# Performance work log

Hardware: AMD Instinct MI355X
Metric: run time of the kernel (lower is better)

The kernel has to match this reference:

```python
import jax, jax.numpy as jnp
import numpy as np

N = 32768      # total nodes
G = 64         # graphs
NPG = 512      # nodes per graph (equal-size graphs)
K = 256        # ceil(NPG * pooling_ratio), pooling_ratio=0.5
D = 256        # input_dim
H = 256        # hidden_dim
FD = 3 * H     # fusion dim
C = 10         # num_classes
E = 262144     # edges
EPS = 1e-5     # BatchNorm eps


def setup_inputs() -> dict:
    key = jax.random.key(0)
    ks = jax.random.split(key, 20)
    w = lambda k, s: jax.random.normal(k, s, jnp.float32) * 0.05
    inp = {
        'x': jax.random.normal(ks[0], (N, D), jnp.float32),
        'edge_index': jax.random.randint(ks[1], (2, E), 0, N, jnp.int64),
        'batch': (jnp.arange(N, dtype=jnp.int64) // NPG),
        'w_s1': w(ks[2], (D, H)), 'b_s1': jnp.zeros((H,), jnp.float32),
        'w_s21': w(ks[3], (D, H)), 'b_s21': jnp.zeros((H,), jnp.float32),
        'w_s22': w(ks[4], (H, H)), 'b_s22': jnp.zeros((H,), jnp.float32),
        'w_raw': w(ks[5], (D, H)), 'b_raw': jnp.zeros((H,), jnp.float32),
        'w_pos': w(ks[6], (FD, 1)), 'b_pos': jnp.zeros((1,), jnp.float32),
        'w_neg': w(ks[7], (FD, 1)), 'b_neg': jnp.zeros((1,), jnp.float32),
        'w_pool': w(ks[8], (FD, FD)), 'b_pool': jnp.zeros((FD,), jnp.float32),
        'w1': w(ks[9], (2 * FD, 256)), 'b1': jnp.zeros((256,), jnp.float32),
        'g1': jnp.ones((256,), jnp.float32), 'be1': jnp.zeros((256,), jnp.float32),
        'w2': w(ks[10], (256, 256)), 'b2': jnp.zeros((256,), jnp.float32),
        'g2': jnp.ones((256,), jnp.float32), 'be2': jnp.zeros((256,), jnp.float32),
        'w3': w(ks[11], (256, 256)), 'b3': jnp.zeros((256,), jnp.float32),
        'g3': jnp.ones((256,), jnp.float32), 'be3': jnp.zeros((256,), jnp.float32),
        'w4': w(ks[12], (256, C)), 'b4': jnp.zeros((C,), jnp.float32),
    }
    return inp


def _gcn(x, W, b, src, dst, dinv):
    # PyG GCNConv: linear, then sym-normalized aggregation with self-loops
    h = x @ W
    norm = dinv[src] * dinv[dst]
    agg = jax.ops.segment_sum(h[src] * norm[:, None], dst, num_segments=N)
    agg = agg + h * (dinv * dinv)[:, None]  # self-loop contribution
    return agg + b


def _bn(z, g, b):
    m = z.mean(0)
    v = z.var(0)  # biased, as torch BN training-mode normalization
    return (z - m) * jax.lax.rsqrt(v + EPS) * g + b


def _mlp(z, w1, b1, g1, be1, w2, b2, g2, be2, w3, b3, g3, be3, w4, b4):
    z = jax.nn.relu(_bn(z @ w1 + b1, g1, be1))  # dropout=identity (eval)
    idt = z
    o = jax.nn.relu(_bn(z @ w2 + b2, g2, be2))
    z = o + idt
    idt = z
    o = jax.nn.relu(_bn(z @ w3 + b3, g3, be3))
    z = o + idt
    return z @ w4 + b4


def _topk_mask(scores):
    # equal-size graphs -> per-graph top-k via one batched lax.top_k
    sg = scores.reshape(G, NPG)
    _, idx = jax.lax.top_k(sg, K)
    mask = jnp.zeros((G, NPG), bool).at[jnp.arange(G)[:, None], idx].set(True)
    return mask.reshape(-1)


def _readout(xt, mask):
    m = mask[:, None]
    xs = jnp.where(m, xt, 0.0).reshape(G, NPG, FD)
    mean_pool = xs.sum(1) / K
    mx = jnp.where(m, xt, -jnp.inf).reshape(G, NPG, FD).max(1)
    return jnp.concatenate([mean_pool, mx], axis=1)


def reference(x, edge_index, batch, w_s1, b_s1, w_s21, b_s21, w_s22, b_s22,
              w_raw, b_raw, w_pos, b_pos, w_neg, b_neg, w_pool, b_pool,
              w1, b1, g1, be1, w2, b2, g2, be2, w3, b3, g3, be3, w4, b4):
    src, dst = edge_index[0], edge_index[1]
    deg = jax.ops.segment_sum(jnp.ones_like(src, jnp.float32), dst, num_segments=N) + 1.0
    dinv = jax.lax.rsqrt(deg)
    lrelu = lambda z: jax.nn.leaky_relu(z, 0.01)

    h_s1 = lrelu(_gcn(x, w_s1, b_s1, src, dst, dinv))
    h_s2 = lrelu(_gcn(lrelu(_gcn(x, w_s21, b_s21, src, dst, dinv)), w_s22, b_s22, src, dst, dinv))
    h_raw = x @ w_raw + b_raw
    h_final = jnp.concatenate([h_s1, h_s2, h_raw], axis=1)  # [N, FD]

    score_pos = jax.nn.sigmoid(_gcn(h_final, w_pos, b_pos, src, dst, dinv)).reshape(-1)
    score_neg = jax.nn.sigmoid(_gcn(h_final, w_neg, b_neg, src, dst, dinv)).reshape(-1)

    xt = jax.nn.sigmoid(h_final @ w_pool + b_pool)  # pool_transform for all nodes; mask selects
    mask_pos = _topk_mask(score_pos)
    mask_neg = _topk_mask(score_neg)

    mlp = lambda e: _mlp(e, w1, b1, g1, be1, w2, b2, g2, be2, w3, b3, g3, be3, w4, b4)
    logits_pos = mlp(_readout(xt, mask_pos))
    probs_pos = jax.nn.softmax(logits_pos, axis=1)
    logits_neg = mlp(_readout(xt, mask_neg))
    probs_neg = jax.nn.softmax(logits_neg, axis=1)
    return (logits_pos, probs_pos, probs_neg, score_pos, score_neg, batch)
```

## Files before the change

kernel.cpp:

```cpp
#include <hip/hip_runtime.h>
#include <hip/hip_bf16.h>

#define N_NODES 32768
#define NGRAPH  64
#define NPG     512
#define TOPK    256
#define HID     256
#define FDIM    768
#define NEDGE   262144
#define NCLS    10
#define BN_EPS  1e-5f

#define IN_BF16 0
#define OUT_BF16 0

typedef __attribute__((ext_vector_type(8))) short short8;
typedef __attribute__((ext_vector_type(4))) float f32x4;

__device__ __forceinline__ float bf2f(unsigned short u) {
    return __uint_as_float(((unsigned)u) << 16);
}
__device__ __forceinline__ unsigned short f2bf(float f) {
    unsigned x = __float_as_uint(f);
    unsigned r = (x + 0x7fffu + ((x >> 16) & 1u)) >> 16;
    return (unsigned short)r;
}
__device__ __forceinline__ float in_ld(const void* p, size_t i) {
#if IN_BF16
    return bf2f(((const unsigned short*)p)[i]);
#else
    return ((const float*)p)[i];
#endif
}
__device__ __forceinline__ void st_out(void* o, size_t i, float v) {
#if OUT_BF16
    ((unsigned short*)o)[i] = f2bf(v);
#else
    ((float*)o)[i] = v;
#endif
}

__device__ __forceinline__ void async_cp16(const unsigned short* g, unsigned short* l) {
    __builtin_amdgcn_global_load_lds(
        (const __attribute__((address_space(1))) unsigned int*)g,
        (__attribute__((address_space(3))) unsigned int*)l, 16, 0, 0);
}

__device__ __forceinline__ void tile_swizzle(int& bm, int& bn) {
    int nx = gridDim.x;
    int L = blockIdx.y * nx + blockIdx.x;
    int xcd = L & 7;
    int j = L >> 3;
    bm = ((j / nx) * 8 + xcd) * 128;
    bn = (j % nx) * 128;
}

__global__ __launch_bounds__(256) void cvt_kernel(const float* __restrict__ in,
                                                  unsigned short* __restrict__ out, int n) {
    int i = blockIdx.x * 256 + threadIdx.x;
    if (i < n) out[i] = f2bf(in[i]);
}

__global__ __launch_bounds__(256) void cvt_t_kernel(const float* __restrict__ in,
                                                    unsigned short* __restrict__ out, int K, int N) {
    __shared__ unsigned short tile[32][33];
    int bk = blockIdx.x * 32, bn = blockIdx.y * 32;
    int tx = threadIdx.x & 31, ty = threadIdx.x >> 5;
#pragma unroll
    for (int i = 0; i < 32; i += 8)
        tile[ty + i][tx] = f2bf(in[(size_t)(bk + ty + i) * N + bn + tx]);
    __syncthreads();
#pragma unroll
    for (int i = 0; i < 32; i += 8)
        out[(size_t)(bn + ty + i) * K + bk + tx] = tile[tx][ty + i];
}

__global__ __launch_bounds__(256) void detect_kernel(const int* __restrict__ eb, int* __restrict__ flag) {
    int i = blockIdx.x * 256 + threadIdx.x;
    int v = eb[2 * (size_t)i + 1];
    unsigned long long b = __ballot(v != 0);
    if ((threadIdx.x & 63) == 0 && b)
        atomicAdd(flag, (int)__popcll(b));
}

__global__ __launch_bounds__(256) void hist_kernel(const int* __restrict__ eb, const int* __restrict__ flag,
                                                   int* __restrict__ deg) {
    int e = blockIdx.x * 256 + threadIdx.x;
    int st = (*flag == 0) ? 2 : 1;
    unsigned d = ((const unsigned*)eb)[(size_t)(NEDGE + e) * st] & (N_NODES - 1);
    atomicAdd(&deg[d], 1);
}

__global__ __launch_bounds__(256) void dinv_kernel(const int* __restrict__ deg, float* __restrict__ dinv) {
    int i = blockIdx.x * 256 + threadIdx.x;
    dinv[i] = rsqrtf((float)deg[i] + 1.0f);
}

__global__ __launch_bounds__(1024) void scan_kernel(const int* __restrict__ cnt, int* __restrict__ rowptr,
                                                    int* __restrict__ cursor) {
    __shared__ int part[1024];
    int t = threadIdx.x;
    int base = t * 32;
    int loc[32];
    int s = 0;
#pragma unroll
    for (int i = 0; i < 32; i++) { loc[i] = cnt[base + i]; s += loc[i]; }
    part[t] = s;
    __syncthreads();
    for (int off = 1; off < 1024; off <<= 1) {
        int v = (t >= off) ? part[t - off] : 0;
        __syncthreads();
        part[t] += v;
        __syncthreads();
    }
    int run = (t == 0) ? 0 : part[t - 1];
#pragma unroll
    for (int i = 0; i < 32; i++) {
        rowptr[base + i] = run;
        cursor[base + i] = run;
        run += loc[i];
    }
    if (t == 1023) rowptr[N_NODES] = run;
}

__global__ __launch_bounds__(256) void scatter_kernel(const int* __restrict__ eb, const int* __restrict__ flag,
                                                      int* __restrict__ cursor, int* __restrict__ srcs) {
    int e = blockIdx.x * 256 + threadIdx.x;
    int st = (*flag == 0) ? 2 : 1;
    unsigned s = ((const unsigned*)eb)[(size_t)e * st] & (N_NODES - 1);
    unsigned d = ((const unsigned*)eb)[(size_t)(NEDGE + e) * st] & (N_NODES - 1);
    int p = atomicAdd(&cursor[d], 1);
    srcs[p] = (int)s;
}

#define GEMM_CORE(K_)                                                           \
    __shared__ unsigned short As[128 * 64];                                     \
    __shared__ unsigned short Bs[128 * 64];                                     \
    const int tid = threadIdx.x;                                                \
    const int wave = tid >> 6;                                                  \
    const int lane = tid & 63;                                                  \
    int bm, bn;                                                                 \
    tile_swizzle(bm, bn);                                                       \
    const int wm = (wave >> 1) * 64;                                            \
    const int wn = (wave & 1) * 64;                                             \
    const int l15 = lane & 15;                                                  \
    const int q = lane >> 4;                                                    \
    f32x4 acc[4][4] = {};                                                       \
    const int srow = lane >> 3;                                                 \
    const int schunk = lane & 7;                                                \
    for (int k0 = 0; k0 < (K_); k0 += 64) {                                     \
        __syncthreads();                                                        \
        _Pragma("unroll")                                                       \
        for (int t = 0; t < 4; t++) {                                           \
            int r = t * 32 + wave * 8 + srow;                                   \
            int gc = schunk ^ (r & 7);                                          \
            const unsigned short* ga = A + (size_t)(bm + r) * (K_) + k0 + gc * 8;\
            const unsigned short* gb = WT + (size_t)(bn + r) * (K_) + k0 + gc * 8;\
            unsigned short* la = &As[(t * 32 + wave * 8) * 64];                 \
            unsigned short* lb = &Bs[(t * 32 + wave * 8) * 64];                 \
            async_cp16(ga, la);                                                 \
            async_cp16(gb, lb);                                                 \
        }                                                                       \
        __syncthreads();                                                        \
        _Pragma("unroll")                                                       \
        for (int h = 0; h < 2; h++) {                                           \
            short8 af[4], bfv[4];                                               \
            int p = (h * 4 + q) ^ (l15 & 7);                                    \
            _Pragma("unroll")                                                   \
            for (int t = 0; t < 4; t++) {                                       \
                int m = wm + t * 16 + l15;                                      \
                int n = wn + t * 16 + l15;                                      \
                af[t] = *(const short8*)&As[m * 64 + p * 8];                    \
                bfv[t] = *(const short8*)&Bs[n * 64 + p * 8];                   \
            }                                                                   \
            _Pragma("unroll")                                                   \
            for (int tm = 0; tm < 4; tm++)                                      \
                _Pragma("unroll")                                               \
                for (int tn = 0; tn < 4; tn++)                                  \
                    acc[tm][tn] = __builtin_amdgcn_mfma_f32_16x16x32_bf16(af[tm], bfv[tn], acc[tm][tn], 0, 0, 0); \
        }                                                                       \
    }

__global__ __launch_bounds__(256) void gemm_kernel(const unsigned short* __restrict__ A,
                                                   const unsigned short* __restrict__ WT,
                                                   const float* __restrict__ bias,
                                                   unsigned short* __restrict__ C,
                                                   int K, int ldC, int colOff, int epi) {
    GEMM_CORE(K)
#pragma unroll
    for (int tm = 0; tm < 4; tm++) {
        int row = bm + wm + tm * 16 + q * 4;
#pragma unroll
        for (int tn = 0; tn < 4; tn++) {
            int col = bn + wn + tn * 16 + l15;
            float bv = bias ? bias[col] : 0.0f;
#pragma unroll
            for (int r = 0; r < 4; r++) {
                float v = acc[tm][tn][r] + bv;
                if (epi == 1) v = 1.0f / (1.0f + __expf(-v));
                C[(size_t)(row + r) * ldC + colOff + col] = f2bf(v);
            }
        }
    }
}

__global__ __launch_bounds__(256) void gemm3_kernel(const unsigned short* __restrict__ A,
                                                    const unsigned short* __restrict__ WT,
                                                    const float* __restrict__ b_raw,
                                                    unsigned short* __restrict__ tA,
                                                    unsigned short* __restrict__ tB,
                                                    unsigned short* __restrict__ hfin) {
    GEMM_CORE(256)
#pragma unroll
    for (int tm = 0; tm < 4; tm++) {
        int row = bm + wm + tm * 16 + q * 4;
#pragma unroll
        for (int tn = 0; tn < 4; tn++) {
            int col = bn + wn + tn * 16 + l15;
            if (col < 256) {
#pragma unroll
                for (int r = 0; r < 4; r++)
                    tA[(size_t)(row + r) * 256 + col] = f2bf(acc[tm][tn][r]);
            } else if (col < 512) {
#pragma unroll
                for (int r = 0; r < 4; r++)
                    tB[(size_t)(row + r) * 256 + (col - 256)] = f2bf(acc[tm][tn][r]);
            } else {
                float bv = b_raw[col - 512];
#pragma unroll
                for (int r = 0; r < 4; r++)
                    hfin[(size_t)(row + r) * 768 + col] = f2bf(acc[tm][tn][r] + bv);
            }
        }
    }
}

__global__ __launch_bounds__(256) void agg_kernel(const unsigned short* __restrict__ h,
                                                  const int* __restrict__ rowptr, const int* __restrict__ srcs,
                                                  const float* __restrict__ dinv, const void* __restrict__ bias,
                                                  unsigned short* __restrict__ out, int ldOut, int colOff,
                                                  int do_lrelu) {
    int wave = threadIdx.x >> 6, lane = threadIdx.x & 63;
    int v = blockIdx.x * 4 + wave;
    int f0 = lane * 4;
    float a0 = 0.f, a1 = 0.f, a2 = 0.f, a3 = 0.f;
    int s = rowptr[v], e = rowptr[v + 1];
    for (int i = s; i < e; i++) {
        int u = srcs[i] & (N_NODES - 1);
        float du = dinv[u];
        uint2 hv = *(const uint2*)(h + (size_t)u * 256 + f0);
        a0 += bf2f((unsigned short)(hv.x & 0xffff)) * du;
        a1 += bf2f((unsigned short)(hv.x >> 16)) * du;
        a2 += bf2f((unsigned short)(hv.y & 0xffff)) * du;
        a3 += bf2f((unsigned short)(hv.y >> 16)) * du;
    }
    float dv = dinv[v], dv2 = dv * dv;
    uint2 sv = *(const uint2*)(h + (size_t)v * 256 + f0);
    float r0 = dv * a0 + bf2f((unsigned short)(sv.x & 0xffff)) * dv2 + in_ld(bias, f0 + 0);
    float r1 = dv * a1 + bf2f((unsigned short)(sv.x >> 16)) * dv2 + in_ld(bias, f0 + 1);
    float r2 = dv * a2 + bf2f((unsigned short)(sv.y & 0xffff)) * dv2 + in_ld(bias, f0 + 2);
    float r3 = dv * a3 + bf2f((unsigned short)(sv.y >> 16)) * dv2 + in_ld(bias, f0 + 3);
    if (do_lrelu) {
        r0 = r0 > 0.f ? r0 : 0.01f * r0;
        r1 = r1 > 0.f ? r1 : 0.01f * r1;
        r2 = r2 > 0.f ? r2 : 0.01f * r2;
        r3 = r3 > 0.f ? r3 : 0.01f * r3;
    }
    unsigned o0 = f2bf(r0), o1 = f2bf(r1), o2 = f2bf(r2), o3 = f2bf(r3);
    uint2 ov = make_uint2((o1 << 16) | o0, (o3 << 16) | o2);
    *(uint2*)(out + (size_t)v * ldOut + colOff + f0) = ov;
}

__global__ __launch_bounds__(256) void score_mv_kernel(const unsigned short* __restrict__ hf,
                                                       const void* __restrict__ wp, const void* __restrict__ wn,
                                                       float* __restrict__ svp, float* __restrict__ svn) {
    int wave = threadIdx.x >> 6, lane = threadIdx.x & 63;
    int v = blockIdx.x * 4 + wave;
    float sp = 0.f, sn = 0.f;
#pragma unroll
    for (int i = 0; i < 3; i++) {
        int k = i * 256 + lane * 4;
        uint2 hv = *(const uint2*)(hf + (size_t)v * 768 + k);
        float x0 = bf2f((unsigned short)(hv.x & 0xffff));
        float x1 = bf2f((unsigned short)(hv.x >> 16));
        float x2 = bf2f((unsigned short)(hv.y & 0xffff));
        float x3 = bf2f((unsigned short)(hv.y >> 16));
        sp += x0 * in_ld(wp, k) + x1 * in_ld(wp, k + 1) + x2 * in_ld(wp, k + 2) + x3 * in_ld(wp, k + 3);
        sn += x0 * in_ld(wn, k) + x1 * in_ld(wn, k + 1) + x2 * in_ld(wn, k + 2) + x3 * in_ld(wn, k + 3);
    }
    for (int off = 32; off >= 1; off >>= 1) {
        sp += __shfl_down(sp, off, 64);
        sn += __shfl_down(sn, off, 64);
    }
    if (lane == 0) { svp[v] = sp; svn[v] = sn; }
}

__global__ __launch_bounds__(256) void score_agg_kernel(const float* __restrict__ svp, const float* __restrict__ svn,
                                                        const int* __restrict__ rowptr, const int* __restrict__ srcs,
                                                        const float* __restrict__ dinv,
                                                        const void* __restrict__ bp, const void* __restrict__ bn_,
                                                        float* __restrict__ scp, float* __restrict__ scn,
                                                        void* __restrict__ dout) {
    int v = blockIdx.x * 256 + threadIdx.x;
    float ap = 0.f, an = 0.f;
    int s = rowptr[v], e = rowptr[v + 1];
    for (int i = s; i < e; i++) {
        int u = srcs[i] & (N_NODES - 1);
        float du = dinv[u];
        ap += svp[u] * du;
        an += svn[u] * du;
    }
    float dv = dinv[v], dv2 = dv * dv;
    float zp = dv * ap + svp[v] * dv2 + in_ld(bp, 0);
    float zn = dv * an + svn[v] * dv2 + in_ld(bn_, 0);
    float pp = 1.0f / (1.0f + __expf(-zp));
    float pn = 1.0f / (1.0f + __expf(-zn));
    scp[v] = pp;
    scn[v] = pn;
    st_out(dout, 1920 + (size_t)v, pp);
    st_out(dout, 1920 + (size_t)N_NODES + v, pn);
}

__global__ __launch_bounds__(512) void topk_kernel(const float* __restrict__ sc, unsigned char* __restrict__ mask) {
    __shared__ float s[512];
    int g = blockIdx.x, i = threadIdx.x;
    float my = sc[(size_t)g * 512 + i];
    s[i] = my;
    __syncthreads();
    int cnt = 0;
    for (int j = 0; j < 512; j++) {
        float o = s[j];
        cnt += (int)((o > my) || ((o == my) && (j < i)));
    }
    mask[(size_t)g * 512 + i] = (cnt < TOPK) ? 1 : 0;
}

__global__ __launch_bounds__(256) void readout2_kernel(const unsigned short* __restrict__ xt,
                                                       const unsigned char* __restrict__ maskp,
                                                       const unsigned char* __restrict__ maskn,
                                                       float* __restrict__ eout) {
    int g = blockIdx.x;
    int c = blockIdx.y;
    int wv = threadIdx.x >> 6, lane = threadIdx.x & 63;
    int f = c * 64 + lane;
    __shared__ unsigned char mp[512], mn[512];
    __shared__ float red[4][64][4];
    for (int i = threadIdx.x; i < 512; i += 256) {
        mp[i] = maskp[(size_t)g * 512 + i];
        mn[i] = maskn[(size_t)g * 512 + i];
    }
    __syncthreads();
    float sp = 0.f, sn = 0.f, xp = -INFINITY, xn = -INFINITY;
    const unsigned short* base = xt + ((size_t)g * 512 + wv * 128) * 768 + f;
    for (int v = 0; v < 128; v++) {
        float x = bf2f(base[(size_t)v * 768]);
        if (mp[wv * 128 + v]) { sp += x; xp = fmaxf(xp, x); }
        if (mn[wv * 128 + v]) { sn += x; xn = fmaxf(xn, x); }
    }
    red[wv][lane][0] = sp; red[wv][lane][1] = xp;
    red[wv][lane][2] = sn; red[wv][lane][3] = xn;
    __syncthreads();
    if (wv == 0) {
#pragma unroll
        for (int w = 1; w < 4; w++) {
            sp += red[w][lane][0]; xp = fmaxf(xp, red[w][lane][1]);
            sn += red[w][lane][2]; xn = fmaxf(xn, red[w][lane][3]);
        }
        float* erp = eout + (size_t)g * 1536;
        float* ern = eout + (size_t)(64 + g) * 1536;
        erp[f] = sp * (1.0f / TOPK);
        erp[768 + f] = xp;
        ern[f] = sn * (1.0f / TOPK);
        ern[768 + f] = xn;
    }
}

__global__ __launch_bounds__(256) void mlp_gemm2_kernel(const float* __restrict__ in,
                                                        const float* __restrict__ W,
                                                        const float* __restrict__ b,
                                                        float* __restrict__ out, int K) {
    __shared__ float row[1536];
    __shared__ float red[4][64];
    int r = blockIdx.x, cg = blockIdx.y;
    int wv = threadIdx.x >> 6, lane = threadIdx.x & 63;
    int c = cg * 64 + lane;
    for (int k = threadIdx.x; k < K; k += 256) row[k] = in[(size_t)r * K + k];
    __syncthreads();
    int kpw = K >> 2;
    const float* wp = W + (size_t)(wv * kpw) * 256 + c;
    const float* rp = row + wv * kpw;
    float acc = 0.f;
#pragma unroll 4
    for (int k = 0; k < kpw; k++)
        acc += rp[k] * wp[(size_t)k * 256];
    red[wv][lane] = acc;
    __syncthreads();
    if (wv == 0) {
        float v = red[0][lane] + red[1][lane] + red[2][lane] + red[3][lane] + b[c];
        out[(size_t)r * 256 + c] = v;
    }
}

__global__ __launch_bounds__(64) void bn_kernel(const float* __restrict__ z, const void* __restrict__ gamma,
                                                const void* __restrict__ beta, const float* __restrict__ res,
                                                float* __restrict__ out) {
    int f = blockIdx.x & 255, g = blockIdx.x >> 8, r = threadIdx.x;
    size_t idx = (size_t)(g * 64 + r) * 256 + f;
    float x = z[idx];
    float s = x, sq = x * x;
    for (int off = 1; off < 64; off <<= 1) {
        s += __shfl_xor(s, off, 64);
        sq += __shfl_xor(sq, off, 64);
    }
    float m = s * (1.0f / 64.0f);
    float var = sq * (1.0f / 64.0f) - m * m;
    float y = (x - m) * rsqrtf(var + BN_EPS) * in_ld(gamma, f) + in_ld(beta, f);
    y = fmaxf(y, 0.0f);
    if (res) y += res[idx];
    out[idx] = y;
}

__global__ __launch_bounds__(64) void logits_kernel(const float* __restrict__ act, const void* __restrict__ w4,
                                                    const void* __restrict__ b4, float* __restrict__ lg) {
    int idx = blockIdx.x * 64 + threadIdx.x;
    if (idx >= 128 * NCLS) return;
    int r = idx / NCLS, c = idx % NCLS;
    float acc = in_ld(b4, c);
    for (int k = 0; k < 256; k++) acc += act[(size_t)r * 256 + k] * in_ld(w4, (size_t)k * NCLS + c);
    lg[idx] = acc;
}

__global__ __launch_bounds__(64) void softmax_kernel(const float* __restrict__ lg, void* __restrict__ dout) {
    int r = blockIdx.x * 64 + threadIdx.x;
    if (r >= 128) return;
    float l[NCLS];
    float mx = -1e30f;
    for (int c = 0; c < NCLS; c++) { l[c] = lg[(size_t)r * NCLS + c]; mx = fmaxf(mx, l[c]); }
    float sum = 0.f;
    float ex[NCLS];
    for (int c = 0; c < NCLS; c++) { ex[c] = __expf(l[c] - mx); sum += ex[c]; }
    float inv = 1.0f / sum;
    int g = r >> 6, rr = r & 63;
    if (g == 0) {
        for (int c = 0; c < NCLS; c++) st_out(dout, (size_t)rr * NCLS + c, l[c]);
        for (int c = 0; c < NCLS; c++) st_out(dout, 640 + (size_t)rr * NCLS + c, ex[c] * inv);
    } else {
        for (int c = 0; c < NCLS; c++) st_out(dout, 1280 + (size_t)rr * NCLS + c, ex[c] * inv);
    }
}

__global__ __launch_bounds__(256) void batch_kernel(void* __restrict__ dout) {
    int i = blockIdx.x * 256 + threadIdx.x;
    st_out(dout, 1920 + 2 * (size_t)N_NODES + i, (float)(i >> 9));
}

extern "C" void kernel_launch(void* const* d_in, const int* in_sizes, int n_in,
                              void* d_out, int out_size, void* d_ws, size_t ws_size,
                              hipStream_t stream) {
    (void)in_sizes; (void)n_in; (void)out_size; (void)ws_size;

    const float* x = (const float*)d_in[0];
    const int* eb = (const int*)d_in[1];
    const float* w_s1 = (const float*)d_in[3];
    const float* b_s1 = (const float*)d_in[4];
    const float* w_s21 = (const float*)d_in[5];
    const float* b_s21 = (const float*)d_in[6];
    const float* w_s22 = (const float*)d_in[7];
    const float* b_s22 = (const float*)d_in[8];
    const float* w_raw = (const float*)d_in[9];
    const float* b_raw = (const float*)d_in[10];
    const void* w_pos = d_in[11];
    const void* b_pos = d_in[12];
    const void* w_neg = d_in[13];
    const void* b_neg = d_in[14];
    const float* w_pool = (const float*)d_in[15];
    const float* b_pool = (const float*)d_in[16];
    const float* w1 = (const float*)d_in[17];  const float* b1 = (const float*)d_in[18];
    const void* g1 = d_in[19];  const void* be1 = d_in[20];
    const float* w2 = (const float*)d_in[21];  const float* b2 = (const float*)d_in[22];
    const void* g2 = d_in[23];  const void* be2 = d_in[24];
    const float* w3 = (const float*)d_in[25];  const float* b3 = (const float*)d_in[26];
    const void* g3 = d_in[27];  const void* be3 = d_in[28];
    const void* w4 = d_in[29];  const void* b4 = d_in[30];

    char* ws = (char*)d_ws;
    size_t off = 0;
    auto alloc = [&](size_t b) -> void* {
        void* p = ws + off;
        off += (b + 255) & ~(size_t)255;
        return p;
    };
    int* flag = (int*)alloc(256);
    int* deg = (int*)alloc((size_t)N_NODES * 4);
    float* dinv = (float*)alloc((size_t)N_NODES * 4);
    int* rowptr = (int*)alloc((size_t)(N_NODES + 1) * 4);
    int* cursor = (int*)alloc((size_t)N_NODES * 4);
    int* srcs = (int*)alloc((size_t)NEDGE * 4);
    unsigned short* xbf = (unsigned short*)alloc((size_t)N_NODES * 256 * 2);
    unsigned short* wcat = (unsigned short*)alloc((size_t)768 * 256 * 2);
    unsigned short* wb_s22 = (unsigned short*)alloc((size_t)256 * 256 * 2);
    unsigned short* wb_pool = (unsigned short*)alloc((size_t)768 * 768 * 2);
    unsigned short* tA = (unsigned short*)alloc((size_t)N_NODES * 256 * 2);
    unsigned short* tB = (unsigned short*)alloc((size_t)N_NODES * 256 * 2);
    unsigned short* tmpB = (unsigned short*)alloc((size_t)N_NODES * 256 * 2);
    unsigned short* hfin = (unsigned short*)alloc((size_t)N_NODES * 768 * 2);
    unsigned short* xt = (unsigned short*)alloc((size_t)N_NODES * 768 * 2);
    float* svp = (float*)alloc((size_t)N_NODES * 4);
    float* svn = (float*)alloc((size_t)N_NODES * 4);
    float* scp = (float*)alloc((size_t)N_NODES * 4);
    float* scn = (float*)alloc((size_t)N_NODES * 4);
    unsigned char* maskp = (unsigned char*)alloc(N_NODES);
    unsigned char* maskn = (unsigned char*)alloc(N_NODES);
    float* ebuf = (float*)alloc((size_t)128 * 1536 * 4);
    float* zb = (float*)alloc((size_t)128 * 256 * 4);
    float* act1 = (float*)alloc((size_t)128 * 256 * 4);
    float* act2 = (float*)alloc((size_t)128 * 256 * 4);
    float* act3 = (float*)alloc((size_t)128 * 256 * 4);
    float* lg = (float*)alloc((size_t)128 * NCLS * 4);

    hipMemsetAsync(flag, 0, 256, stream);
    hipMemsetAsync(deg, 0, (size_t)N_NODES * 4, stream);
    detect_kernel<<<NEDGE / 256, 256, 0, stream>>>(eb, flag);
    hist_kernel<<<NEDGE / 256, 256, 0, stream>>>(eb, flag, deg);
    dinv_kernel<<<N_NODES / 256, 256, 0, stream>>>(deg, dinv);
    scan_kernel<<<1, 1024, 0, stream>>>(deg, rowptr, cursor);
    scatter_kernel<<<NEDGE / 256, 256, 0, stream>>>(eb, flag, cursor, srcs);

    cvt_kernel<<<(N_NODES * 256 + 255) / 256, 256, 0, stream>>>(x, xbf, N_NODES * 256);
    {
        dim3 g8(8, 8), g24(24, 24);
        cvt_t_kernel<<<g8, 256, 0, stream>>>(w_s1, wcat, 256, 256);
        cvt_t_kernel<<<g8, 256, 0, stream>>>(w_s21, wcat + (size_t)256 * 256, 256, 256);
        cvt_t_kernel<<<g8, 256, 0, stream>>>(w_raw, wcat + (size_t)512 * 256, 256, 256);
        cvt_t_kernel<<<g8, 256, 0, stream>>>(w_s22, wb_s22, 256, 256);
        cvt_t_kernel<<<g24, 256, 0, stream>>>(w_pool, wb_pool, 768, 768);
    }

    dim3 gG3(768 / 128, N_NODES / 128);
    dim3 gA(256 / 128, N_NODES / 128);
    dim3 gP(768 / 128, N_NODES / 128);

    gemm3_kernel<<<gG3, 256, 0, stream>>>(xbf, wcat, b_raw, tA, tB, hfin);
    agg_kernel<<<N_NODES / 4, 256, 0, stream>>>(tA, rowptr, srcs, dinv, b_s1, hfin, 768, 0, 1);
    agg_kernel<<<N_NODES / 4, 256, 0, stream>>>(tB, rowptr, srcs, dinv, b_s21, tmpB, 256, 0, 1);
    gemm_kernel<<<gA, 256, 0, stream>>>(tmpB, wb_s22, nullptr, tA, 256, 256, 0, 0);
    agg_kernel<<<N_NODES / 4, 256, 0, stream>>>(tA, rowptr, srcs, dinv, b_s22, hfin, 768, 256, 1);
    gemm_kernel<<<gP, 256, 0, stream>>>(hfin, wb_pool, b_pool, xt, 768, 768, 0, 1);
    score_mv_kernel<<<N_NODES / 4, 256, 0, stream>>>(hfin, w_pos, w_neg, svp, svn);
    score_agg_kernel<<<N_NODES / 256, 256, 0, stream>>>(svp, svn, rowptr, srcs, dinv, b_pos, b_neg, scp, scn, d_out);
    topk_kernel<<<NGRAPH, 512, 0, stream>>>(scp, maskp);
    topk_kernel<<<NGRAPH, 512, 0, stream>>>(scn, maskn);
    {
        dim3 gR(NGRAPH, FDIM / 64);
        readout2_kernel<<<gR, 256, 0, stream>>>(xt, maskp, maskn, ebuf);
    }
    {
        dim3 gM(128, 4);
        mlp_gemm2_kernel<<<gM, 256, 0, stream>>>(ebuf, w1, b1, zb, 1536);
        bn_kernel<<<512, 64, 0, stream>>>(zb, g1, be1, nullptr, act1);
        mlp_gemm2_kernel<<<gM, 256, 0, stream>>>(act1, w2, b2, zb, 256);
        bn_kernel<<<512, 64, 0, stream>>>(zb, g2, be2, act1, act2);
        mlp_gemm2_kernel<<<gM, 256, 0, stream>>>(act2, w3, b3, zb, 256);
        bn_kernel<<<512, 64, 0, stream>>>(zb, g3, be3, act2, act3);
    }
    logits_kernel<<<(128 * NCLS + 63) / 64, 64, 0, stream>>>(act3, w4, b4, lg);
    softmax_kernel<<<2, 64, 0, stream>>>(lg, d_out);
    batch_kernel<<<N_NODES / 256, 256, 0, stream>>>(d_out);
}
```

Measured before the change: 627.4 us.

## Fuse small launches, merge paired aggregations, template GEMM K, skip unmasked readout rows

Several unrelated changes land together. The five weight-transpose launches become one kernel, dinv is computed inside the scan, the batch output is written by the score kernel, and the two top-k launches become one. The first two GCN aggregations are fused so each neighbour's index and dinv are read once for both feature sets. gemm_kernel takes K as a template parameter so its loop can be unrolled, and the readout skips loading xt rows that neither mask selects. The goal is less launch overhead and less redundant memory traffic, at the cost of more register pressure in the fused aggregation kernel.

New measurement: 603.5 us. -3.8%, faster.

```diff
diff --git a/kernel.cpp b/kernel.cpp
--- a/kernel.cpp
+++ b/kernel.cpp
@@ -61,18 +61,34 @@
     if (i < n) out[i] = f2bf(in[i]);
 }
 
-__global__ __launch_bounds__(256) void cvt_t_kernel(const float* __restrict__ in,
-                                                    unsigned short* __restrict__ out, int K, int N) {
+__global__ __launch_bounds__(256) void cvt_t_all_kernel(const float* __restrict__ w_s1,
+                                                        const float* __restrict__ w_s21,
+                                                        const float* __restrict__ w_raw,
+                                                        const float* __restrict__ w_s22,
+                                                        const float* __restrict__ w_pool,
+                                                        unsigned short* __restrict__ wcat,
+                                                        unsigned short* __restrict__ wb_s22,
+                                                        unsigned short* __restrict__ wb_pool) {
     __shared__ unsigned short tile[32][33];
-    int bk = blockIdx.x * 32, bn = blockIdx.y * 32;
+    int id = blockIdx.x;
+    const float* src;
+    unsigned short* dst;
+    int K, N, t;
+    if (id < 64)       { src = w_s1;  dst = wcat;                       K = 256; N = 256; t = id; }
+    else if (id < 128) { src = w_s21; dst = wcat + (size_t)256 * 256;   K = 256; N = 256; t = id - 64; }
+    else if (id < 192) { src = w_raw; dst = wcat + (size_t)512 * 256;   K = 256; N = 256; t = id - 128; }
+    else if (id < 256) { src = w_s22; dst = wb_s22;                     K = 256; N = 256; t = id - 192; }
+    else               { src = w_pool; dst = wb_pool;                   K = 768; N = 768; t = id - 256; }
+    int tiles_x = K >> 5;
+    int bk = (t % tiles_x) * 32, bn = (t / tiles_x) * 32;
     int tx = threadIdx.x & 31, ty = threadIdx.x >> 5;
 #pragma unroll
     for (int i = 0; i < 32; i += 8)
-        tile[ty + i][tx] = f2bf(in[(size_t)(bk + ty + i) * N + bn + tx]);
+        tile[ty + i][tx] = f2bf(src[(size_t)(bk + ty + i) * N + bn + tx]);
     __syncthreads();
 #pragma unroll
     for (int i = 0; i < 32; i += 8)
-        out[(size_t)(bn + ty + i) * K + bk + tx] = tile[tx][ty + i];
+        dst[(size_t)(bn + ty + i) * K + bk + tx] = tile[tx][ty + i];
 }
 
 __global__ __launch_bounds__(256) void detect_kernel(const int* __restrict__ eb, int* __restrict__ flag) {
@@ -91,13 +107,8 @@
     atomicAdd(&deg[d], 1);
 }
 
-__global__ __launch_bounds__(256) void dinv_kernel(const int* __restrict__ deg, float* __restrict__ dinv) {
-    int i = blockIdx.x * 256 + threadIdx.x;
-    dinv[i] = rsqrtf((float)deg[i] + 1.0f);
-}
-
 __global__ __launch_bounds__(1024) void scan_kernel(const int* __restrict__ cnt, int* __restrict__ rowptr,
-                                                    int* __restrict__ cursor) {
+                                                    int* __restrict__ cursor, float* __restrict__ dinv) {
     __shared__ int part[1024];
     int t = threadIdx.x;
     int base = t * 32;
@@ -118,6 +129,7 @@
     for (int i = 0; i < 32; i++) {
         rowptr[base + i] = run;
         cursor[base + i] = run;
+        dinv[base + i] = rsqrtf((float)loc[i] + 1.0f);
         run += loc[i];
     }
     if (t == 1023) rowptr[N_NODES] = run;
@@ -181,12 +193,13 @@
         }                                                                       \
     }
 
+template <int K_>
 __global__ __launch_bounds__(256) void gemm_kernel(const unsigned short* __restrict__ A,
                                                    const unsigned short* __restrict__ WT,
                                                    const float* __restrict__ bias,
                                                    unsigned short* __restrict__ C,
-                                                   int K, int ldC, int colOff, int epi) {
-    GEMM_CORE(K)
+                                                   int ldC, int colOff, int epi) {
+    GEMM_CORE(K_)
 #pragma unroll
     for (int tm = 0; tm < 4; tm++) {
         int row = bm + wm + tm * 16 + q * 4;
@@ -235,9 +248,57 @@
     }
 }
 
+__global__ __launch_bounds__(256) void agg2_kernel(const unsigned short* __restrict__ hA,
+                                                   const unsigned short* __restrict__ hB,
+                                                   const int* __restrict__ rowptr, const int* __restrict__ srcs,
+                                                   const float* __restrict__ dinv,
+                                                   const float* __restrict__ biasA, const float* __restrict__ biasB,
+                                                   unsigned short* __restrict__ outA,
+                                                   unsigned short* __restrict__ outB) {
+    int wave = threadIdx.x >> 6, lane = threadIdx.x & 63;
+    int v = blockIdx.x * 4 + wave;
+    int f0 = lane * 4;
+    float a0 = 0.f, a1 = 0.f, a2 = 0.f, a3 = 0.f;
+    float c0 = 0.f, c1 = 0.f, c2 = 0.f, c3 = 0.f;
+    int s = rowptr[v], e = rowptr[v + 1];
+    for (int i = s; i < e; i++) {
+        int u = srcs[i] & (N_NODES - 1);
+        float du = dinv[u];
+        uint2 ha = *(const uint2*)(hA + (size_t)u * 256 + f0);
+        uint2 hb = *(const uint2*)(hB + (size_t)u * 256 + f0);
+        a0 += bf2f((unsigned short)(ha.x & 0xffff)) * du;
+        a1 += bf2f((unsigned short)(ha.x >> 16)) * du;
+        a2 += bf2f((unsigned short)(ha.y & 0xffff)) * du;
+        a3 += bf2f((unsigned short)(ha.y >> 16)) * du;
+        c0 += bf2f((unsigned short)(hb.x & 0xffff)) * du;
+        c1 += bf2f((unsigned short)(hb.x >> 16)) * du;
+        c2 += bf2f((unsigned short)(hb.y & 0xffff)) * du;
+        c3 += bf2f((unsigned short)(hb.y >> 16)) * du;
+    }
+    float dv = dinv[v], dv2 = dv * dv;
+    uint2 sa = *(const uint2*)(hA + (size_t)v * 256 + f0);
+    uint2 sb = *(const uint2*)(hB + (size_t)v * 256 + f0);
+    float r0 = dv * a0 + bf2f((unsigned short)(sa.x & 0xffff)) * dv2 + biasA[f0 + 0];
+    float r1 = dv * a1 + bf2f((unsigned short)(sa.x >> 16)) * dv2 + biasA[f0 + 1];
+    float r2 = dv * a2 + bf2f((unsigned short)(sa.y & 0xffff)) * dv2 + biasA[f0 + 2];
+    float r3 = dv * a3 + bf2f((unsigned short)(sa.y >> 16)) * dv2 + biasA[f0 + 3];
+    float t0 = dv * c0 + bf2f((unsigned short)(sb.x & 0xffff)) * dv2 + biasB[f0 + 0];
+    float t1 = dv * c1 + bf2f((unsigned short)(sb.x >> 16)) * dv2 + biasB[f0 + 1];
+    float t2 = dv * c2 + bf2f((unsigned short)(sb.y & 0xffff)) * dv2 + biasB[f0 + 2];
+    float t3 = dv * c3 + bf2f((unsigned short)(sb.y >> 16)) * dv2 + biasB[f0 + 3];
+    r0 = r0 > 0.f ? r0 : 0.01f * r0;  r1 = r1 > 0.f ? r1 : 0.01f * r1;
+    r2 = r2 > 0.f ? r2 : 0.01f * r2;  r3 = r3 > 0.f ? r3 : 0.01f * r3;
+    t0 = t0 > 0.f ? t0 : 0.01f * t0;  t1 = t1 > 0.f ? t1 : 0.01f * t1;
+    t2 = t2 > 0.f ? t2 : 0.01f * t2;  t3 = t3 > 0.f ? t3 : 0.01f * t3;
+    uint2 ov = make_uint2(((unsigned)f2bf(r1) << 16) | f2bf(r0), ((unsigned)f2bf(r3) << 16) | f2bf(r2));
+    uint2 ow = make_uint2(((unsigned)f2bf(t1) << 16) | f2bf(t0), ((unsigned)f2bf(t3) << 16) | f2bf(t2));
+    *(uint2*)(outA + (size_t)v * 768 + f0) = ov;
+    *(uint2*)(outB + (size_t)v * 256 + f0) = ow;
+}
+
 __global__ __launch_bounds__(256) void agg_kernel(const unsigned short* __restrict__ h,
                                                   const int* __restrict__ rowptr, const int* __restrict__ srcs,
-                                                  const float* __restrict__ dinv, const void* __restrict__ bias,
+                                                  const float* __restrict__ dinv, const float* __restrict__ bias,
                                                   unsigned short* __restrict__ out, int ldOut, int colOff,
                                                   int do_lrelu) {
     int wave = threadIdx.x >> 6, lane = threadIdx.x & 63;
@@ -256,18 +317,17 @@
     }
     float dv = dinv[v], dv2 = dv * dv;
     uint2 sv = *(const uint2*)(h + (size_t)v * 256 + f0);
-    float r0 = dv * a0 + bf2f((unsigned short)(sv.x & 0xffff)) * dv2 + in_ld(bias, f0 + 0);
-    float r1 = dv * a1 + bf2f((unsigned short)(sv.x >> 16)) * dv2 + in_ld(bias, f0 + 1);
-    float r2 = dv * a2 + bf2f((unsigned short)(sv.y & 0xffff)) * dv2 + in_ld(bias, f0 + 2);
-    float r3 = dv * a3 + bf2f((unsigned short)(sv.y >> 16)) * dv2 + in_ld(bias, f0 + 3);
+    float r0 = dv * a0 + bf2f((unsigned short)(sv.x & 0xffff)) * dv2 + bias[f0 + 0];
+    float r1 = dv * a1 + bf2f((unsigned short)(sv.x >> 16)) * dv2 + bias[f0 + 1];
+    float r2 = dv * a2 + bf2f((unsigned short)(sv.y & 0xffff)) * dv2 + bias[f0 + 2];
+    float r3 = dv * a3 + bf2f((unsigned short)(sv.y >> 16)) * dv2 + bias[f0 + 3];
     if (do_lrelu) {
         r0 = r0 > 0.f ? r0 : 0.01f * r0;
         r1 = r1 > 0.f ? r1 : 0.01f * r1;
         r2 = r2 > 0.f ? r2 : 0.01f * r2;
         r3 = r3 > 0.f ? r3 : 0.01f * r3;
     }
-    unsigned o0 = f2bf(r0), o1 = f2bf(r1), o2 = f2bf(r2), o3 = f2bf(r3);
-    uint2 ov = make_uint2((o1 << 16) | o0, (o3 << 16) | o2);
+    uint2 ov = make_uint2(((unsigned)f2bf(r1) << 16) | f2bf(r0), ((unsigned)f2bf(r3) << 16) | f2bf(r2));
     *(uint2*)(out + (size_t)v * ldOut + colOff + f0) = ov;
 }
 
@@ -319,11 +379,16 @@
     scn[v] = pn;
     st_out(dout, 1920 + (size_t)v, pp);
     st_out(dout, 1920 + (size_t)N_NODES + v, pn);
-}
-
-__global__ __launch_bounds__(512) void topk_kernel(const float* __restrict__ sc, unsigned char* __restrict__ mask) {
+    st_out(dout, 1920 + 2 * (size_t)N_NODES + v, (float)(v >> 9));
+}
+
+__global__ __launch_bounds__(512) void topk2_kernel(const float* __restrict__ scp, const float* __restrict__ scn,
+                                                    unsigned char* __restrict__ maskp,
+                                                    unsigned char* __restrict__ maskn) {
     __shared__ float s[512];
-    int g = blockIdx.x, i = threadIdx.x;
+    const float* sc = (blockIdx.x & 1) ? scn : scp;
+    unsigned char* mask = (blockIdx.x & 1) ? maskn : maskp;
+    int g = blockIdx.x >> 1, i = threadIdx.x;
     float my = sc[(size_t)g * 512 + i];
     s[i] = my;
     __syncthreads();
@@ -353,9 +418,11 @@
     float sp = 0.f, sn = 0.f, xp = -INFINITY, xn = -INFINITY;
     const unsigned short* base = xt + ((size_t)g * 512 + wv * 128) * 768 + f;
     for (int v = 0; v < 128; v++) {
+        unsigned char bp = mp[wv * 128 + v], bn_ = mn[wv * 128 + v];
+        if (!(bp | bn_)) continue;
         float x = bf2f(base[(size_t)v * 768]);
-        if (mp[wv * 128 + v]) { sp += x; xp = fmaxf(xp, x); }
-        if (mn[wv * 128 + v]) { sn += x; xn = fmaxf(xn, x); }
+        if (bp) { sp += x; xp = fmaxf(xp, x); }
+        if (bn_) { sn += x; xn = fmaxf(xn, x); }
     }
     red[wv][lane][0] = sp; red[wv][lane][1] = xp;
     red[wv][lane][2] = sn; red[wv][lane][3] = xn;
@@ -447,11 +514,6 @@
     } else {
         for (int c = 0; c < NCLS; c++) st_out(dout, 1280 + (size_t)rr * NCLS + c, ex[c] * inv);
     }
-}
-
-__global__ __launch_bounds__(256) void batch_kernel(void* __restrict__ dout) {
-    int i = blockIdx.x * 256 + threadIdx.x;
-    st_out(dout, 1920 + 2 * (size_t)N_NODES + i, (float)(i >> 9));
 }
 
 extern "C" void kernel_launch(void* const* d_in, const int* in_sizes, int n_in,
@@ -522,34 +584,24 @@
     hipMemsetAsync(deg, 0, (size_t)N_NODES * 4, stream);
     detect_kernel<<<NEDGE / 256, 256, 0, stream>>>(eb, flag);
     hist_kernel<<<NEDGE / 256, 256, 0, stream>>>(eb, flag, deg);
-    dinv_kernel<<<N_NODES / 256, 256, 0, stream>>>(deg, dinv);
-    scan_kernel<<<1, 1024, 0, stream>>>(deg, rowptr, cursor);
+    scan_kernel<<<1, 1024, 0, stream>>>(deg, rowptr, cursor, dinv);
     scatter_kernel<<<NEDGE / 256, 256, 0, stream>>>(eb, flag, cursor, srcs);
 
     cvt_kernel<<<(N_NODES * 256 + 255) / 256, 256, 0, stream>>>(x, xbf, N_NODES * 256);
-    {
-        dim3 g8(8, 8), g24(24, 24);
-        cvt_t_kernel<<<g8, 256, 0, stream>>>(w_s1, wcat, 256, 256);
-        cvt_t_kernel<<<g8, 256, 0, stream>>>(w_s21, wcat + (size_t)256 * 256, 256, 256);
-        cvt_t_kernel<<<g8, 256, 0, stream>>>(w_raw, wcat + (size_t)512 * 256, 256, 256);
-        cvt_t_kernel<<<g8, 256, 0, stream>>>(w_s22, wb_s22, 256, 256);
-        cvt_t_kernel<<<g24, 256, 0, stream>>>(w_pool, wb_pool, 768, 768);
-    }
+    cvt_t_all_kernel<<<832, 256, 0, stream>>>(w_s1, w_s21, w_raw, w_s22, w_pool, wcat, wb_s22, wb_pool);
 
     dim3 gG3(768 / 128, N_NODES / 128);
     dim3 gA(256 / 128, N_NODES / 128);
     dim3 gP(768 / 128, N_NODES / 128);
 
     gemm3_kernel<<<gG3, 256, 0, stream>>>(xbf, wcat, b_raw, tA, tB, hfin);
-    agg_kernel<<<N_NODES / 4, 256, 0, stream>>>(tA, rowptr, srcs, dinv, b_s1, hfin, 768, 0, 1);
-    agg_kernel<<<N_NODES / 4, 256, 0, stream>>>(tB, rowptr, srcs, dinv, b_s21, tmpB, 256, 0, 1);
-    gemm_kernel<<<gA, 256, 0, stream>>>(tmpB, wb_s22, nullptr, tA, 256, 256, 0, 0);
+    agg2_kernel<<<N_NODES / 4, 256, 0, stream>>>(tA, tB, rowptr, srcs, dinv, b_s1, b_s21, hfin, tmpB);
+    gemm_kernel<256><<<gA, 256, 0, stream>>>(tmpB, wb_s22, nullptr, tA, 256, 0, 0);
     agg_kernel<<<N_NODES / 4, 256, 0, stream>>>(tA, rowptr, srcs, dinv, b_s22, hfin, 768, 256, 1);
-    gemm_kernel<<<gP, 256, 0, stream>>>(hfin, wb_pool, b_pool, xt, 768, 768, 0, 1);
+    gemm_kernel<768><<<gP, 256, 0, stream>>>(hfin, wb_pool, b_pool, xt, 768, 0, 1);
     score_mv_kernel<<<N_NODES / 4, 256, 0, stream>>>(hfin, w_pos, w_neg, svp, svn);
     score_agg_kernel<<<N_NODES / 256, 256, 0, stream>>>(svp, svn, rowptr, srcs, dinv, b_pos, b_neg, scp, scn, d_out);
-    topk_kernel<<<NGRAPH, 512, 0, stream>>>(scp, maskp);
-    topk_kernel<<<NGRAPH, 512, 0, stream>>>(scn, maskn);
+    topk2_kernel<<<2 * NGRAPH, 512, 0, stream>>>(scp, scn, maskp, maskn);
     {
         dim3 gR(NGRAPH, FDIM / 64);
         readout2_kernel<<<gR, 256, 0, stream>>>(xt, maskp, maskn, ebuf);
@@ -565,5 +617,4 @@
     }
     logits_kernel<<<(128 * NCLS + 63) / 64, 64, 0, stream>>>(act3, w4, b4, lg);
     softmax_kernel<<<2, 64, 0, stream>>>(lg, d_out);
-    batch_kernel<<<N_NODES / 256, 256, 0, stream>>>(d_out);
-}
+}
```
